# Kernel optimization log

Hardware: AMD Instinct MI355X
Metric: run time of the kernel (lower is better)

Reference implementation:

```python
import jax, jax.numpy as jnp
import numpy as np

IN_FEATURES = 4096
OUT_FEATURES = 4096
KERNEL_SIZE = 4  # MaxPool1d stride defaults to kernel_size
SCALE = 0.5


def setup_inputs() -> dict:
    key = jax.random.key(0)
    kx, kw, kb = jax.random.split(key, 3)
    bound = 1.0 / np.sqrt(IN_FEATURES)
    x = jax.random.normal(kx, (4096, IN_FEATURES), dtype=jnp.float32)
    W = jax.random.uniform(kw, (OUT_FEATURES, IN_FEATURES), dtype=jnp.float32, minval=-bound, maxval=bound)
    b = jax.random.uniform(kb, (OUT_FEATURES,), dtype=jnp.float32, minval=-bound, maxval=bound)
    return {"x": x, "W": W, "b": b}


def reference(x, W, b) -> jnp.ndarray:
    # Linear: [B, I] @ [I, O] + [O] -> [B, O]
    y = jnp.einsum("bi,oi->bo", x, W) + b
    B, O = y.shape
    K = KERNEL_SIZE
    n_win = (O - K) // K + 1  # stride == kernel_size, no padding
    # Non-overlapping window max-pool: [B, n_win, K] -> max over K
    pooled = y[:, : n_win * K].reshape(B, n_win, K).max(axis=-1)
    # Sum over pooled dim, then scale -> [B]
    return pooled.sum(axis=-1) * SCALE
```

## Files before the change

### kernel.cpp

```cpp
#include <hip/hip_runtime.h>
#include <hip/hip_bf16.h>

#define KDIM 4096
#define NTILE 64
#define NELEM16 (1u << 24)

typedef float f32x4 __attribute__((ext_vector_type(4)));
typedef short bf16x8 __attribute__((ext_vector_type(8)));

typedef const __attribute__((address_space(1))) unsigned int g_u32;
typedef __attribute__((address_space(3))) unsigned int l_u32;

__device__ __forceinline__ void gload_lds16(const void* g, void* l) {
    __builtin_amdgcn_global_load_lds((g_u32*)g, (l_u32*)l, 16, 0, 0);
}

__device__ __forceinline__ unsigned int pack_bf16x2(float lo, float hi) {
    __hip_bfloat162 h = __float22bfloat162_rn(float2{lo, hi});
    union { __hip_bfloat162 h; unsigned int u; } c; c.h = h; return c.u;
}

__global__ __launch_bounds__(256)
void pack_swz(const float* __restrict__ in, unsigned short* __restrict__ out)
{
    const unsigned int stride = gridDim.x * blockDim.x;
    for (unsigned int i = blockIdx.x * blockDim.x + threadIdx.x; i < (1u << 21); i += stride) {
        const unsigned int cp = i & 7;
        const unsigned int rl = (i >> 3) & 127;
        const unsigned int c  = cp ^ (rl & 7);
        const unsigned int h  = (i >> 10) & 1;
        const unsigned int kt = (i >> 11) & 63;
        const unsigned int rt = i >> 17;
        const unsigned int row = rt * 256 + h * 128 + rl;
        const unsigned int col = kt * 64 + c * 8;
        const float4* s = (const float4*)(in + (size_t)row * KDIM + col);
        const float4 a = s[0], b = s[1];
        uint4 o;
        o.x = pack_bf16x2(a.x, a.y); o.y = pack_bf16x2(a.z, a.w);
        o.z = pack_bf16x2(b.x, b.y); o.w = pack_bf16x2(b.z, b.w);
        *(uint4*)(out + (size_t)i * 8) = o;
    }
}

#define STAGE(matBase, kt, h, bufp, opIdx)                                      \
    {                                                                           \
        const unsigned short* g_ = (matBase) + ((size_t)(kt) * 2 + (h)) * 8192; \
        const unsigned int lo_ = (bufp) * 32768 + (opIdx) * 16384 + (h) * 8192 + wid * 1024; \
        gload_lds16(g_ + stageOff,       &lds[lo_]);                            \
        gload_lds16(g_ + stageOff + 512, &lds[lo_ + 512]);                      \
    }

#define PHASE(P, MFB, NFB, STAGE_STMT, VMSTMT)                                  \
    {                                                                           \
        bf16x8 af[4][2], bfr[2][2];                                             \
        _Pragma("unroll") for (int m = 0; m < 2; ++m)                           \
          _Pragma("unroll") for (int k = 0; k < 2; ++k)                         \
            af[m][k] = *(const bf16x8*)&lds[(P) * 32768 + (((MFB) + m) >> 2) * 8192 + \
                ((((MFB) + m) & 3) * 2 + wm) * 1024 + rdBase + kcp[k]];         \
        _Pragma("unroll") for (int m = 2; m < 4; ++m)                           \
          _Pragma("unroll") for (int k = 0; k < 2; ++k)                         \
            af[m][k] = *(const bf16x8*)&lds[(P) * 32768 + (((MFB) + m) >> 2) * 8192 + \
                ((((MFB) + m) & 3) * 2 + wm) * 1024 + rdBase + kcp[k]];         \
        _Pragma("unroll") for (int n = 0; n < 2; ++n)                           \
          _Pragma("unroll") for (int k = 0; k < 2; ++k)                         \
            bfr[n][k] = *(const bf16x8*)&lds[(P) * 32768 + 16384 +              \
                (((NFB) + n) >> 1) * 8192 + ((((NFB) + n) & 1) * 4 + wn) * 1024 + rdBase + kcp[k]]; \
        STAGE_STMT;                                                             \
        __builtin_amdgcn_s_barrier();                                           \
        __builtin_amdgcn_s_setprio(1);                                          \
        _Pragma("unroll") for (int m = 0; m < 4; ++m)                           \
          _Pragma("unroll") for (int n = 0; n < 2; ++n)                         \
            _Pragma("unroll") for (int k = 0; k < 2; ++k)                       \
              acc[(MFB) + m][(NFB) + n] = __builtin_amdgcn_mfma_f32_16x16x32_bf16( \
                  af[m][k], bfr[n][k], acc[(MFB) + m][(NFB) + n], 0, 0, 0);     \
        __builtin_amdgcn_s_setprio(0);                                          \
        VMSTMT;                                                                 \
        __builtin_amdgcn_s_barrier();                                           \
    }

__global__ __launch_bounds__(512, 2)
void gemm_8phase(const unsigned short* __restrict__ A,
                 const unsigned short* __restrict__ B,
                 const float* __restrict__ bias,
                 float* __restrict__ out)
{
    __shared__ unsigned short lds[65536];

    const int tid  = threadIdx.x;
    const int lane = tid & 63;
    const int wid  = tid >> 6;
    const int wm   = wid >> 2;
    const int wn   = wid & 3;
    const int c15  = lane & 15;
    const int q4   = lane >> 4;
    const int c7   = c15 & 7;

    const int bid = blockIdx.x;
    const int wg  = (bid & 7) * 32 + (bid >> 3);
    const int bm  = wg >> 4;
    const int bn  = wg & 15;

    const unsigned short* Abase = A + (size_t)bm * 64 * 2 * 8192;
    const unsigned short* Bbase = B + (size_t)bn * 64 * 2 * 8192;

    const int stageOff = wid * 1024 + lane * 8;
    const int rdBase   = c15 * 64;
    const int kcp[2]   = { ((0 + q4) ^ c7) * 8, ((4 + q4) ^ c7) * 8 };

    f32x4 acc[8][4];
    #pragma unroll
    for (int i = 0; i < 8; ++i)
        #pragma unroll
        for (int j = 0; j < 4; ++j)
            acc[i][j] = (f32x4)0.0f;

    STAGE(Abase, 0, 0, 0, 0);
    STAGE(Abase, 0, 1, 0, 0);
    STAGE(Bbase, 0, 0, 0, 1);
    STAGE(Bbase, 0, 1, 0, 1);
    STAGE(Bbase, 1, 0, 1, 1);
    STAGE(Abase, 1, 1, 1, 0);
    asm volatile("s_waitcnt vmcnt(4)" ::: "memory");
    __builtin_amdgcn_s_barrier();

    #pragma unroll 2
    for (int t = 0; t < NTILE; ++t) {
        const int p = t & 1;
        PHASE(p, 0, 0, if (t + 1 < NTILE) STAGE(Abase, t + 1, 0, p ^ 1, 0), );
        PHASE(p, 4, 0, if (t + 1 < NTILE) STAGE(Bbase, t + 1, 1, p ^ 1, 1), );
        PHASE(p, 4, 2, if (t + 2 < NTILE) STAGE(Bbase, t + 2, 0, p, 1), );
        PHASE(p, 0, 2, if (t + 2 < NTILE) STAGE(Abase, t + 2, 1, p, 0),
              if (t < NTILE - 2) { asm volatile("s_waitcnt vmcnt(4)" ::: "memory"); }
              else               { asm volatile("s_waitcnt vmcnt(0)" ::: "memory"); });
    }

    float rs[8][4];
    #pragma unroll
    for (int mf = 0; mf < 8; ++mf)
        #pragma unroll
        for (int r = 0; r < 4; ++r)
            rs[mf][r] = 0.0f;

    #pragma unroll
    for (int nf = 0; nf < 4; ++nf) {
        const float bv = bias[bn * 256 + (nf * 4 + wn) * 16 + c15];
        #pragma unroll
        for (int mf = 0; mf < 8; ++mf) {
            #pragma unroll
            for (int r = 0; r < 4; ++r) {
                float v = acc[mf][nf][r] + bv;
                v = fmaxf(v, __shfl_xor(v, 1));
                v = fmaxf(v, __shfl_xor(v, 2));
                v += __shfl_xor(v, 4);
                v += __shfl_xor(v, 8);
                rs[mf][r] += v;
            }
        }
    }

    if (c15 == 0) {
        #pragma unroll
        for (int mf = 0; mf < 8; ++mf)
            #pragma unroll
            for (int r = 0; r < 4; ++r) {
                const int row = bm * 256 + (mf * 2 + wm) * 16 + q4 * 4 + r;
                atomicAdd(&out[row], 0.5f * rs[mf][r]);
            }
    }
}

__global__ __launch_bounds__(256, 2)
void fused_gemm_pool_fallback(const float* __restrict__ x,
                              const float* __restrict__ W,
                              const float* __restrict__ b,
                              float* __restrict__ out)
{
    __shared__ unsigned short As[128][72];
    __shared__ unsigned short Bs[128][72];

    const int tid  = threadIdx.x;
    const int lane = tid & 63;
    const int wid  = tid >> 6;
    const int wm   = wid >> 1;
    const int wn   = wid & 1;

    const int bid = blockIdx.x;
    const int wg  = (bid & 7) * 128 + (bid >> 3);
    const int bm  = wg >> 5;
    const int bn  = wg & 31;

    const int srow = tid >> 4;
    const int scol = tid & 15;

    const float* xbase = x + (size_t)(bm * 128 + srow) * KDIM + scol * 4;
    const float* wbase = W + (size_t)(bn * 128 + srow) * KDIM + scol * 4;

    f32x4 acc[4][4];
    #pragma unroll
    for (int i = 0; i < 4; ++i)
        #pragma unroll
        for (int j = 0; j < 4; ++j)
            acc[i][j] = (f32x4)0.0f;

    float4 ra[8], rb[8];
    #pragma unroll
    for (int p = 0; p < 8; ++p) {
        ra[p] = *(const float4*)(xbase + (size_t)(p * 16) * KDIM);
        rb[p] = *(const float4*)(wbase + (size_t)(p * 16) * KDIM);
    }

    for (int kt = 0; kt < KDIM / 64; ++kt) {
        #pragma unroll
        for (int p = 0; p < 8; ++p) {
            const int r = srow + p * 16;
            uint2 pa, pb;
            pa.x = pack_bf16x2(ra[p].x, ra[p].y);
            pa.y = pack_bf16x2(ra[p].z, ra[p].w);
            pb.x = pack_bf16x2(rb[p].x, rb[p].y);
            pb.y = pack_bf16x2(rb[p].z, rb[p].w);
            *(uint2*)&As[r][scol * 4] = pa;
            *(uint2*)&Bs[r][scol * 4] = pb;
        }
        __syncthreads();

        if (kt + 1 < KDIM / 64) {
            const float* xa = xbase + (size_t)(kt + 1) * 64;
            const float* wa = wbase + (size_t)(kt + 1) * 64;
            #pragma unroll
            for (int p = 0; p < 8; ++p) {
                ra[p] = *(const float4*)(xa + (size_t)(p * 16) * KDIM);
                rb[p] = *(const float4*)(wa + (size_t)(p * 16) * KDIM);
            }
        }

        #pragma unroll
        for (int k0 = 0; k0 < 2; ++k0) {
            const int kk = k0 * 32 + (lane >> 4) * 8;
            bf16x8 af[4], bfr[4];
            #pragma unroll
            for (int mf = 0; mf < 4; ++mf)
                af[mf] = *(const bf16x8*)&As[wm * 64 + mf * 16 + (lane & 15)][kk];
            #pragma unroll
            for (int nf = 0; nf < 4; ++nf)
                bfr[nf] = *(const bf16x8*)&Bs[wn * 64 + nf * 16 + (lane & 15)][kk];
            #pragma unroll
            for (int mf = 0; mf < 4; ++mf)
                #pragma unroll
                for (int nf = 0; nf < 4; ++nf)
                    acc[mf][nf] = __builtin_amdgcn_mfma_f32_16x16x32_bf16(
                        af[mf], bfr[nf], acc[mf][nf], 0, 0, 0);
        }
        __syncthreads();
    }

    float rs[4][4];
    #pragma unroll
    for (int mf = 0; mf < 4; ++mf)
        #pragma unroll
        for (int r = 0; r < 4; ++r)
            rs[mf][r] = 0.0f;

    #pragma unroll
    for (int nf = 0; nf < 4; ++nf) {
        const float bv = b[bn * 128 + wn * 64 + nf * 16 + (lane & 15)];
        #pragma unroll
        for (int mf = 0; mf < 4; ++mf) {
            #pragma unroll
            for (int r = 0; r < 4; ++r) {
                float v = acc[mf][nf][r] + bv;
                v = fmaxf(v, __shfl_xor(v, 1));
                v = fmaxf(v, __shfl_xor(v, 2));
                v += __shfl_xor(v, 4);
                v += __shfl_xor(v, 8);
                rs[mf][r] += v;
            }
        }
    }

    if ((lane & 15) == 0) {
        #pragma unroll
        for (int mf = 0; mf < 4; ++mf)
            #pragma unroll
            for (int r = 0; r < 4; ++r) {
                const int row = bm * 128 + wm * 64 + mf * 16 + (lane >> 4) * 4 + r;
                atomicAdd(&out[row], 0.5f * rs[mf][r]);
            }
    }
}

extern "C" void kernel_launch(void* const* d_in, const int* in_sizes, int n_in,
                              void* d_out, int out_size, void* d_ws, size_t ws_size,
                              hipStream_t stream) {
    const float* x = (const float*)d_in[0];
    const float* W = (const float*)d_in[1];
    const float* b = (const float*)d_in[2];
    float* out = (float*)d_out;

    hipMemsetAsync(out, 0, (size_t)out_size * sizeof(float), stream);

    const size_t need = (size_t)NELEM16 * 2 * sizeof(unsigned short);
    if (ws_size >= need) {
        unsigned short* xb = (unsigned short*)d_ws;
        unsigned short* wb = xb + (size_t)NELEM16;
        pack_swz<<<dim3(2048), dim3(256), 0, stream>>>(x, xb);
        pack_swz<<<dim3(2048), dim3(256), 0, stream>>>(W, wb);
        gemm_8phase<<<dim3(256), dim3(512), 0, stream>>>(xb, wb, b, out);
    } else {
        fused_gemm_pool_fallback<<<dim3(1024), dim3(256), 0, stream>>>(x, W, b, out);
    }
}
```

Baseline: 187.9 us.

## Reuse LDS fragments across GEMM phases and fuse the two pack kernels

The four-phase main loop now keeps A and B fragments in registers across phases, so each phase loads only one new operand half (A0+B0, then B1, then A1, then nothing) instead of reloading both A and B every phase. This cuts LDS read traffic per tile and the matching waits. The x and W bf16 pack kernels are merged into a single launch, saving one launch and its tail. The catch is more live vector registers for the fragments under a 512-thread, 2-block launch bound, which risks spills or lower occupancy.

```diff
diff --git a/kernel.cpp b/kernel.cpp
--- a/kernel.cpp
+++ b/kernel.cpp
@@ -21,16 +21,20 @@
 }
 
 __global__ __launch_bounds__(256)
-void pack_swz(const float* __restrict__ in, unsigned short* __restrict__ out)
+void pack_swz2(const float* __restrict__ x, const float* __restrict__ W,
+               unsigned short* __restrict__ xb, unsigned short* __restrict__ wb)
 {
     const unsigned int stride = gridDim.x * blockDim.x;
-    for (unsigned int i = blockIdx.x * blockDim.x + threadIdx.x; i < (1u << 21); i += stride) {
-        const unsigned int cp = i & 7;
-        const unsigned int rl = (i >> 3) & 127;
+    for (unsigned int i = blockIdx.x * blockDim.x + threadIdx.x; i < (1u << 22); i += stride) {
+        const unsigned int j  = i & ((1u << 21) - 1);
+        const float* __restrict__ in = (i >> 21) ? W : x;
+        unsigned short* __restrict__ out = (i >> 21) ? wb : xb;
+        const unsigned int cp = j & 7;
+        const unsigned int rl = (j >> 3) & 127;
         const unsigned int c  = cp ^ (rl & 7);
-        const unsigned int h  = (i >> 10) & 1;
-        const unsigned int kt = (i >> 11) & 63;
-        const unsigned int rt = i >> 17;
+        const unsigned int h  = (j >> 10) & 1;
+        const unsigned int kt = (j >> 11) & 63;
+        const unsigned int rt = j >> 17;
         const unsigned int row = rt * 256 + h * 128 + rl;
         const unsigned int col = kt * 64 + c * 8;
         const float4* s = (const float4*)(in + (size_t)row * KDIM + col);
@@ -38,7 +42,7 @@
         uint4 o;
         o.x = pack_bf16x2(a.x, a.y); o.y = pack_bf16x2(a.z, a.w);
         o.z = pack_bf16x2(b.x, b.y); o.w = pack_bf16x2(b.z, b.w);
-        *(uint4*)(out + (size_t)i * 8) = o;
+        *(uint4*)(out + (size_t)j * 8) = o;
     }
 }
 
@@ -48,34 +52,6 @@
         const unsigned int lo_ = (bufp) * 32768 + (opIdx) * 16384 + (h) * 8192 + wid * 1024; \
         gload_lds16(g_ + stageOff,       &lds[lo_]);                            \
         gload_lds16(g_ + stageOff + 512, &lds[lo_ + 512]);                      \
-    }
-
-#define PHASE(P, MFB, NFB, STAGE_STMT, VMSTMT)                                  \
-    {                                                                           \
-        bf16x8 af[4][2], bfr[2][2];                                             \
-        _Pragma("unroll") for (int m = 0; m < 2; ++m)                           \
-          _Pragma("unroll") for (int k = 0; k < 2; ++k)                         \
-            af[m][k] = *(const bf16x8*)&lds[(P) * 32768 + (((MFB) + m) >> 2) * 8192 + \
-                ((((MFB) + m) & 3) * 2 + wm) * 1024 + rdBase + kcp[k]];         \
-        _Pragma("unroll") for (int m = 2; m < 4; ++m)                           \
-          _Pragma("unroll") for (int k = 0; k < 2; ++k)                         \
-            af[m][k] = *(const bf16x8*)&lds[(P) * 32768 + (((MFB) + m) >> 2) * 8192 + \
-                ((((MFB) + m) & 3) * 2 + wm) * 1024 + rdBase + kcp[k]];         \
-        _Pragma("unroll") for (int n = 0; n < 2; ++n)                           \
-          _Pragma("unroll") for (int k = 0; k < 2; ++k)                         \
-            bfr[n][k] = *(const bf16x8*)&lds[(P) * 32768 + 16384 +              \
-                (((NFB) + n) >> 1) * 8192 + ((((NFB) + n) & 1) * 4 + wn) * 1024 + rdBase + kcp[k]]; \
-        STAGE_STMT;                                                             \
-        __builtin_amdgcn_s_barrier();                                           \
-        __builtin_amdgcn_s_setprio(1);                                          \
-        _Pragma("unroll") for (int m = 0; m < 4; ++m)                           \
-          _Pragma("unroll") for (int n = 0; n < 2; ++n)                         \
-            _Pragma("unroll") for (int k = 0; k < 2; ++k)                       \
-              acc[(MFB) + m][(NFB) + n] = __builtin_amdgcn_mfma_f32_16x16x32_bf16( \
-                  af[m][k], bfr[n][k], acc[(MFB) + m][(NFB) + n], 0, 0, 0);     \
-        __builtin_amdgcn_s_setprio(0);                                          \
-        VMSTMT;                                                                 \
-        __builtin_amdgcn_s_barrier();                                           \
     }
 
 __global__ __launch_bounds__(512, 2)
@@ -114,6 +90,10 @@
         for (int j = 0; j < 4; ++j)
             acc[i][j] = (f32x4)0.0f;
 
+    bf16x8 afr[4][2];
+    bf16x8 b0f[2][2];
+    bf16x8 b1f[2][2];
+
     STAGE(Abase, 0, 0, 0, 0);
     STAGE(Abase, 0, 1, 0, 0);
     STAGE(Bbase, 0, 0, 0, 1);
@@ -125,13 +105,86 @@
 
     #pragma unroll 2
     for (int t = 0; t < NTILE; ++t) {
-        const int p = t & 1;
-        PHASE(p, 0, 0, if (t + 1 < NTILE) STAGE(Abase, t + 1, 0, p ^ 1, 0), );
-        PHASE(p, 4, 0, if (t + 1 < NTILE) STAGE(Bbase, t + 1, 1, p ^ 1, 1), );
-        PHASE(p, 4, 2, if (t + 2 < NTILE) STAGE(Bbase, t + 2, 0, p, 1), );
-        PHASE(p, 0, 2, if (t + 2 < NTILE) STAGE(Abase, t + 2, 1, p, 0),
-              if (t < NTILE - 2) { asm volatile("s_waitcnt vmcnt(4)" ::: "memory"); }
-              else               { asm volatile("s_waitcnt vmcnt(0)" ::: "memory"); });
+        const int p  = t & 1;
+        const int pb = p * 32768;
+
+        #pragma unroll
+        for (int m = 0; m < 4; ++m)
+            #pragma unroll
+            for (int k = 0; k < 2; ++k)
+                afr[m][k] = *(const bf16x8*)&lds[pb + (m * 2 + wm) * 1024 + rdBase + kcp[k]];
+        #pragma unroll
+        for (int n = 0; n < 2; ++n)
+            #pragma unroll
+            for (int k = 0; k < 2; ++k)
+                b0f[n][k] = *(const bf16x8*)&lds[pb + 16384 + (n * 4 + wn) * 1024 + rdBase + kcp[k]];
+        if (t + 1 < NTILE) STAGE(Abase, t + 1, 0, p ^ 1, 0);
+        __builtin_amdgcn_s_barrier();
+        __builtin_amdgcn_s_setprio(1);
+        #pragma unroll
+        for (int m = 0; m < 4; ++m)
+            #pragma unroll
+            for (int n = 0; n < 2; ++n)
+                #pragma unroll
+                for (int k = 0; k < 2; ++k)
+                    acc[m][n] = __builtin_amdgcn_mfma_f32_16x16x32_bf16(
+                        afr[m][k], b0f[n][k], acc[m][n], 0, 0, 0);
+        __builtin_amdgcn_s_setprio(0);
+        __builtin_amdgcn_s_barrier();
+
+        #pragma unroll
+        for (int n = 0; n < 2; ++n)
+            #pragma unroll
+            for (int k = 0; k < 2; ++k)
+                b1f[n][k] = *(const bf16x8*)&lds[pb + 16384 + 8192 + (n * 4 + wn) * 1024 + rdBase + kcp[k]];
+        if (t + 1 < NTILE) STAGE(Bbase, t + 1, 1, p ^ 1, 1);
+        __builtin_amdgcn_s_barrier();
+        __builtin_amdgcn_s_setprio(1);
+        #pragma unroll
+        for (int m = 0; m < 4; ++m)
+            #pragma unroll
+            for (int n = 0; n < 2; ++n)
+                #pragma unroll
+                for (int k = 0; k < 2; ++k)
+                    acc[m][2 + n] = __builtin_amdgcn_mfma_f32_16x16x32_bf16(
+                        afr[m][k], b1f[n][k], acc[m][2 + n], 0, 0, 0);
+        __builtin_amdgcn_s_setprio(0);
+        __builtin_amdgcn_s_barrier();
+
+        #pragma unroll
+        for (int m = 0; m < 4; ++m)
+            #pragma unroll
+            for (int k = 0; k < 2; ++k)
+                afr[m][k] = *(const bf16x8*)&lds[pb + 8192 + (m * 2 + wm) * 1024 + rdBase + kcp[k]];
+        if (t + 2 < NTILE) STAGE(Bbase, t + 2, 0, p, 1);
+        __builtin_amdgcn_s_barrier();
+        __builtin_amdgcn_s_setprio(1);
+        #pragma unroll
+        for (int m = 0; m < 4; ++m)
+            #pragma unroll
+            for (int n = 0; n < 2; ++n)
+                #pragma unroll
+                for (int k = 0; k < 2; ++k)
+                    acc[4 + m][2 + n] = __builtin_amdgcn_mfma_f32_16x16x32_bf16(
+                        afr[m][k], b1f[n][k], acc[4 + m][2 + n], 0, 0, 0);
+        __builtin_amdgcn_s_setprio(0);
+        __builtin_amdgcn_s_barrier();
+
+        if (t + 2 < NTILE) STAGE(Abase, t + 2, 1, p, 0);
+        __builtin_amdgcn_s_barrier();
+        __builtin_amdgcn_s_setprio(1);
+        #pragma unroll
+        for (int m = 0; m < 4; ++m)
+            #pragma unroll
+            for (int n = 0; n < 2; ++n)
+                #pragma unroll
+                for (int k = 0; k < 2; ++k)
+                    acc[4 + m][n] = __builtin_amdgcn_mfma_f32_16x16x32_bf16(
+                        afr[m][k], b0f[n][k], acc[4 + m][n], 0, 0, 0);
+        __builtin_amdgcn_s_setprio(0);
+        if (t < NTILE - 2) { asm volatile("s_waitcnt vmcnt(4)" ::: "memory"); }
+        else               { asm volatile("s_waitcnt vmcnt(0)" ::: "memory"); }
+        __builtin_amdgcn_s_barrier();
     }
 
     float rs[8][4];
@@ -302,8 +355,7 @@
     if (ws_size >= need) {
         unsigned short* xb = (unsigned short*)d_ws;
         unsigned short* wb = xb + (size_t)NELEM16;
-        pack_swz<<<dim3(2048), dim3(256), 0, stream>>>(x, xb);
-        pack_swz<<<dim3(2048), dim3(256), 0, stream>>>(W, wb);
+        pack_swz2<<<dim3(2048), dim3(256), 0, stream>>>(x, W, xb, wb);
         gemm_8phase<<<dim3(256), dim3(512), 0, stream>>>(xb, wb, b, out);
     } else {
         fused_gemm_pool_fallback<<<dim3(1024), dim3(256), 0, stream>>>(x, W, b, out);
```

After: 170.9 us. 1.1x faster.

## Software-pipeline LDS fragment reads across phases and merge pack kernels

Applied to the files above, without the earlier changes.

Restructures the GEMM main loop so LDS fragment reads for the next phase are issued before the current phase's MFMAs. Fragment registers are double-buffered (aA/aB, b0A/b0B), fine-grained lgkmcnt waits and sched_barriers are used, and the prefetch distance of global-to-LDS staging changes to two tiles ahead. This aims to hide LDS read latency behind matrix work. It also fuses the two bf16 pack launches into one kernel to save a launch. The trade-off is higher register pressure and tricky buffer-reuse correctness.

```diff
diff --git a/kernel.cpp b/kernel.cpp
--- a/kernel.cpp
+++ b/kernel.cpp
@@ -21,16 +21,20 @@
 }
 
 __global__ __launch_bounds__(256)
-void pack_swz(const float* __restrict__ in, unsigned short* __restrict__ out)
+void pack_swz2(const float* __restrict__ x, const float* __restrict__ W,
+               unsigned short* __restrict__ xb, unsigned short* __restrict__ wb)
 {
     const unsigned int stride = gridDim.x * blockDim.x;
-    for (unsigned int i = blockIdx.x * blockDim.x + threadIdx.x; i < (1u << 21); i += stride) {
-        const unsigned int cp = i & 7;
-        const unsigned int rl = (i >> 3) & 127;
+    for (unsigned int i = blockIdx.x * blockDim.x + threadIdx.x; i < (1u << 22); i += stride) {
+        const unsigned int j  = i & ((1u << 21) - 1);
+        const float* __restrict__ in = (i >> 21) ? W : x;
+        unsigned short* __restrict__ out = (i >> 21) ? wb : xb;
+        const unsigned int cp = j & 7;
+        const unsigned int rl = (j >> 3) & 127;
         const unsigned int c  = cp ^ (rl & 7);
-        const unsigned int h  = (i >> 10) & 1;
-        const unsigned int kt = (i >> 11) & 63;
-        const unsigned int rt = i >> 17;
+        const unsigned int h  = (j >> 10) & 1;
+        const unsigned int kt = (j >> 11) & 63;
+        const unsigned int rt = j >> 17;
         const unsigned int row = rt * 256 + h * 128 + rl;
         const unsigned int col = kt * 64 + c * 8;
         const float4* s = (const float4*)(in + (size_t)row * KDIM + col);
@@ -38,7 +42,7 @@
         uint4 o;
         o.x = pack_bf16x2(a.x, a.y); o.y = pack_bf16x2(a.z, a.w);
         o.z = pack_bf16x2(b.x, b.y); o.w = pack_bf16x2(b.z, b.w);
-        *(uint4*)(out + (size_t)i * 8) = o;
+        *(uint4*)(out + (size_t)j * 8) = o;
     }
 }
 
@@ -50,31 +54,60 @@
         gload_lds16(g_ + stageOff + 512, &lds[lo_ + 512]);                      \
     }
 
-#define PHASE(P, MFB, NFB, STAGE_STMT, VMSTMT)                                  \
+#define READ_A(dst, base)                                                       \
+    _Pragma("unroll") for (int m = 0; m < 4; ++m)                               \
+      _Pragma("unroll") for (int k = 0; k < 2; ++k)                             \
+        dst[m][k] = *(const bf16x8*)&lds[(base) + (m * 2 + wm) * 1024 + rdBase + kcp[k]];
+
+#define READ_B(dst, base)                                                       \
+    _Pragma("unroll") for (int n = 0; n < 2; ++n)                               \
+      _Pragma("unroll") for (int k = 0; k < 2; ++k)                             \
+        dst[n][k] = *(const bf16x8*)&lds[(base) + (n * 4 + wn) * 1024 + rdBase + kcp[k]];
+
+#define MFMA16(AF, BF, MO, NO)                                                  \
+    __builtin_amdgcn_s_setprio(1);                                              \
+    _Pragma("unroll") for (int m = 0; m < 4; ++m)                               \
+      _Pragma("unroll") for (int n = 0; n < 2; ++n)                             \
+        _Pragma("unroll") for (int k = 0; k < 2; ++k)                           \
+          acc[(MO) + m][(NO) + n] = __builtin_amdgcn_mfma_f32_16x16x32_bf16(    \
+              AF[m][k], BF[n][k], acc[(MO) + m][(NO) + n], 0, 0, 0);            \
+    __builtin_amdgcn_s_setprio(0);
+
+#define TILE_BODY(t, PB, B0CUR, B0NXT)                                          \
     {                                                                           \
-        bf16x8 af[4][2], bfr[2][2];                                             \
-        _Pragma("unroll") for (int m = 0; m < 2; ++m)                           \
-          _Pragma("unroll") for (int k = 0; k < 2; ++k)                         \
-            af[m][k] = *(const bf16x8*)&lds[(P) * 32768 + (((MFB) + m) >> 2) * 8192 + \
-                ((((MFB) + m) & 3) * 2 + wm) * 1024 + rdBase + kcp[k]];         \
-        _Pragma("unroll") for (int m = 2; m < 4; ++m)                           \
-          _Pragma("unroll") for (int k = 0; k < 2; ++k)                         \
-            af[m][k] = *(const bf16x8*)&lds[(P) * 32768 + (((MFB) + m) >> 2) * 8192 + \
-                ((((MFB) + m) & 3) * 2 + wm) * 1024 + rdBase + kcp[k]];         \
-        _Pragma("unroll") for (int n = 0; n < 2; ++n)                           \
-          _Pragma("unroll") for (int k = 0; k < 2; ++k)                         \
-            bfr[n][k] = *(const bf16x8*)&lds[(P) * 32768 + 16384 +              \
-                (((NFB) + n) >> 1) * 8192 + ((((NFB) + n) & 1) * 4 + wn) * 1024 + rdBase + kcp[k]]; \
-        STAGE_STMT;                                                             \
-        __builtin_amdgcn_s_barrier();                                           \
-        __builtin_amdgcn_s_setprio(1);                                          \
-        _Pragma("unroll") for (int m = 0; m < 4; ++m)                           \
-          _Pragma("unroll") for (int n = 0; n < 2; ++n)                         \
-            _Pragma("unroll") for (int k = 0; k < 2; ++k)                       \
-              acc[(MFB) + m][(NFB) + n] = __builtin_amdgcn_mfma_f32_16x16x32_bf16( \
-                  af[m][k], bfr[n][k], acc[(MFB) + m][(NFB) + n], 0, 0, 0);     \
-        __builtin_amdgcn_s_setprio(0);                                          \
-        VMSTMT;                                                                 \
+                                                                        \
+        READ_B(b1, (PB) + 16384 + 8192);                                        \
+        asm volatile("s_waitcnt lgkmcnt(4)" ::: "memory");                      \
+        __builtin_amdgcn_sched_barrier(0);                                      \
+        if ((t) + 2 < NTILE) STAGE(Abase, (t) + 2, 0, (PB) ? 1 : 0, 0);         \
+        __builtin_amdgcn_s_barrier();                                           \
+        MFMA16(aA, B0CUR, 0, 0);                                                \
+        __builtin_amdgcn_s_barrier();                                           \
+                                                                        \
+        READ_A(aB, (PB) + 8192);                                                \
+        asm volatile("s_waitcnt lgkmcnt(8)" ::: "memory");                      \
+        __builtin_amdgcn_sched_barrier(0);                                      \
+        if ((t) + 2 < NTILE) STAGE(Bbase, (t) + 2, 0, (PB) ? 1 : 0, 1);         \
+        __builtin_amdgcn_s_barrier();                                           \
+        MFMA16(aA, b1, 0, 2);                                                   \
+        __builtin_amdgcn_s_barrier();                                           \
+                                                                        \
+        READ_A(aA, (PB) ^ 32768);                                               \
+        asm volatile("s_waitcnt lgkmcnt(8)" ::: "memory");                      \
+        __builtin_amdgcn_sched_barrier(0);                                      \
+        if ((t) + 2 < NTILE) STAGE(Bbase, (t) + 2, 1, (PB) ? 1 : 0, 1);         \
+        __builtin_amdgcn_s_barrier();                                           \
+        MFMA16(aB, b1, 4, 2);                                                   \
+        __builtin_amdgcn_s_barrier();                                           \
+                                                                        \
+        READ_B(B0NXT, ((PB) ^ 32768) + 16384);                                  \
+        asm volatile("s_waitcnt lgkmcnt(4)" ::: "memory");                      \
+        __builtin_amdgcn_sched_barrier(0);                                      \
+        if ((t) + 2 < NTILE) STAGE(Abase, (t) + 2, 1, (PB) ? 1 : 0, 0);         \
+        __builtin_amdgcn_s_barrier();                                           \
+        MFMA16(aB, B0CUR, 4, 0);                                                \
+        if ((t) < NTILE - 2)       { asm volatile("s_waitcnt vmcnt(4)" ::: "memory"); } \
+        else if ((t) == NTILE - 2) { asm volatile("s_waitcnt vmcnt(0)" ::: "memory"); } \
         __builtin_amdgcn_s_barrier();                                           \
     }
 
@@ -114,24 +147,29 @@
         for (int j = 0; j < 4; ++j)
             acc[i][j] = (f32x4)0.0f;
 
+    bf16x8 aA[4][2];
+    bf16x8 aB[4][2];
+    bf16x8 b1[2][2];
+    bf16x8 b0A[2][2];
+    bf16x8 b0B[2][2];
+
     STAGE(Abase, 0, 0, 0, 0);
-    STAGE(Abase, 0, 1, 0, 0);
     STAGE(Bbase, 0, 0, 0, 1);
     STAGE(Bbase, 0, 1, 0, 1);
+    STAGE(Abase, 0, 1, 0, 0);
+    STAGE(Abase, 1, 0, 1, 0);
     STAGE(Bbase, 1, 0, 1, 1);
+    STAGE(Bbase, 1, 1, 1, 1);
     STAGE(Abase, 1, 1, 1, 0);
     asm volatile("s_waitcnt vmcnt(4)" ::: "memory");
     __builtin_amdgcn_s_barrier();
 
-    #pragma unroll 2
-    for (int t = 0; t < NTILE; ++t) {
-        const int p = t & 1;
-        PHASE(p, 0, 0, if (t + 1 < NTILE) STAGE(Abase, t + 1, 0, p ^ 1, 0), );
-        PHASE(p, 4, 0, if (t + 1 < NTILE) STAGE(Bbase, t + 1, 1, p ^ 1, 1), );
-        PHASE(p, 4, 2, if (t + 2 < NTILE) STAGE(Bbase, t + 2, 0, p, 1), );
-        PHASE(p, 0, 2, if (t + 2 < NTILE) STAGE(Abase, t + 2, 1, p, 0),
-              if (t < NTILE - 2) { asm volatile("s_waitcnt vmcnt(4)" ::: "memory"); }
-              else               { asm volatile("s_waitcnt vmcnt(0)" ::: "memory"); });
+    READ_A(aA,  0);
+    READ_B(b0A, 16384);
+
+    for (int tt = 0; tt < NTILE; tt += 2) {
+        TILE_BODY(tt,     0,     b0A, b0B);
+        TILE_BODY(tt + 1, 32768, b0B, b0A);
     }
 
     float rs[8][4];
@@ -302,8 +340,7 @@
     if (ws_size >= need) {
         unsigned short* xb = (unsigned short*)d_ws;
         unsigned short* wb = xb + (size_t)NELEM16;
-        pack_swz<<<dim3(2048), dim3(256), 0, stream>>>(x, xb);
-        pack_swz<<<dim3(2048), dim3(256), 0, stream>>>(W, wb);
+        pack_swz2<<<dim3(2048), dim3(256), 0, stream>>>(x, W, xb, wb);
         gemm_8phase<<<dim3(256), dim3(512), 0, stream>>>(xb, wb, b, out);
     } else {
         fused_gemm_pool_fallback<<<dim3(1024), dim3(256), 0, stream>>>(x, W, b, out);
```

Result: slower. 195.0 us (+3.8%).

## Pre-pack operands in MFMA fragment order and load directly to registers, dropping LDS

Applied to the files above, without the earlier changes.

The pack kernel now writes x and W in the exact per-lane MFMA fragment order and handles both matrices in one launch. The GEMM drops LDS staging and barriers entirely: each wave loads its fragments straight from global memory into registers, double-buffered across K half-tiles. This removes LDS traffic and synchronisation, but each wave now fetches its own A/B fragments from global/L2 with less data reuse across waves. Register pressure also rises, and occupancy is reduced to one block per CU.

```diff
diff --git a/kernel.cpp b/kernel.cpp
--- a/kernel.cpp
+++ b/kernel.cpp
@@ -8,84 +8,58 @@
 typedef float f32x4 __attribute__((ext_vector_type(4)));
 typedef short bf16x8 __attribute__((ext_vector_type(8)));
 
-typedef const __attribute__((address_space(1))) unsigned int g_u32;
-typedef __attribute__((address_space(3))) unsigned int l_u32;
-
-__device__ __forceinline__ void gload_lds16(const void* g, void* l) {
-    __builtin_amdgcn_global_load_lds((g_u32*)g, (l_u32*)l, 16, 0, 0);
-}
-
 __device__ __forceinline__ unsigned int pack_bf16x2(float lo, float hi) {
     __hip_bfloat162 h = __float22bfloat162_rn(float2{lo, hi});
     union { __hip_bfloat162 h; unsigned int u; } c; c.h = h; return c.u;
 }
 
 __global__ __launch_bounds__(256)
-void pack_swz(const float* __restrict__ in, unsigned short* __restrict__ out)
+void pack_frag2(const float* __restrict__ x, const float* __restrict__ W,
+                unsigned short* __restrict__ xb, unsigned short* __restrict__ wb)
 {
     const unsigned int stride = gridDim.x * blockDim.x;
-    for (unsigned int i = blockIdx.x * blockDim.x + threadIdx.x; i < (1u << 21); i += stride) {
-        const unsigned int cp = i & 7;
-        const unsigned int rl = (i >> 3) & 127;
-        const unsigned int c  = cp ^ (rl & 7);
-        const unsigned int h  = (i >> 10) & 1;
-        const unsigned int kt = (i >> 11) & 63;
-        const unsigned int rt = i >> 17;
-        const unsigned int row = rt * 256 + h * 128 + rl;
-        const unsigned int col = kt * 64 + c * 8;
-        const float4* s = (const float4*)(in + (size_t)row * KDIM + col);
-        const float4 a = s[0], b = s[1];
+    for (unsigned int i = blockIdx.x * blockDim.x + threadIdx.x; i < (1u << 22); i += stride) {
+        const unsigned int j  = i & ((1u << 21) - 1);
+        const float* __restrict__ in = (i >> 21) ? W : x;
+        unsigned short* __restrict__ out = (i >> 21) ? wb : xb;
+        const unsigned int lane = j & 63;
+        const unsigned int s    = (j >> 6) & 1;
+        const unsigned int f    = (j >> 7) & 15;
+        const unsigned int kt   = (j >> 11) & 63;
+        const unsigned int t    = j >> 17;
+        const unsigned int row  = t * 256 + f * 16 + (lane & 15);
+        const unsigned int col  = kt * 64 + s * 32 + (lane >> 4) * 8;
+        const float4* sp = (const float4*)(in + (size_t)row * KDIM + col);
+        const float4 a = sp[0], b = sp[1];
         uint4 o;
         o.x = pack_bf16x2(a.x, a.y); o.y = pack_bf16x2(a.z, a.w);
         o.z = pack_bf16x2(b.x, b.y); o.w = pack_bf16x2(b.z, b.w);
-        *(uint4*)(out + (size_t)i * 8) = o;
-    }
-}
-
-#define STAGE(matBase, kt, h, bufp, opIdx)                                      \
-    {                                                                           \
-        const unsigned short* g_ = (matBase) + ((size_t)(kt) * 2 + (h)) * 8192; \
-        const unsigned int lo_ = (bufp) * 32768 + (opIdx) * 16384 + (h) * 8192 + wid * 1024; \
-        gload_lds16(g_ + stageOff,       &lds[lo_]);                            \
-        gload_lds16(g_ + stageOff + 512, &lds[lo_ + 512]);                      \
-    }
-
-#define PHASE(P, MFB, NFB, STAGE_STMT, VMSTMT)                                  \
-    {                                                                           \
-        bf16x8 af[4][2], bfr[2][2];                                             \
-        _Pragma("unroll") for (int m = 0; m < 2; ++m)                           \
-          _Pragma("unroll") for (int k = 0; k < 2; ++k)                         \
-            af[m][k] = *(const bf16x8*)&lds[(P) * 32768 + (((MFB) + m) >> 2) * 8192 + \
-                ((((MFB) + m) & 3) * 2 + wm) * 1024 + rdBase + kcp[k]];         \
-        _Pragma("unroll") for (int m = 2; m < 4; ++m)                           \
-          _Pragma("unroll") for (int k = 0; k < 2; ++k)                         \
-            af[m][k] = *(const bf16x8*)&lds[(P) * 32768 + (((MFB) + m) >> 2) * 8192 + \
-                ((((MFB) + m) & 3) * 2 + wm) * 1024 + rdBase + kcp[k]];         \
-        _Pragma("unroll") for (int n = 0; n < 2; ++n)                           \
-          _Pragma("unroll") for (int k = 0; k < 2; ++k)                         \
-            bfr[n][k] = *(const bf16x8*)&lds[(P) * 32768 + 16384 +              \
-                (((NFB) + n) >> 1) * 8192 + ((((NFB) + n) & 1) * 4 + wn) * 1024 + rdBase + kcp[k]]; \
-        STAGE_STMT;                                                             \
-        __builtin_amdgcn_s_barrier();                                           \
-        __builtin_amdgcn_s_setprio(1);                                          \
-        _Pragma("unroll") for (int m = 0; m < 4; ++m)                           \
-          _Pragma("unroll") for (int n = 0; n < 2; ++n)                         \
-            _Pragma("unroll") for (int k = 0; k < 2; ++k)                       \
-              acc[(MFB) + m][(NFB) + n] = __builtin_amdgcn_mfma_f32_16x16x32_bf16( \
-                  af[m][k], bfr[n][k], acc[(MFB) + m][(NFB) + n], 0, 0, 0);     \
-        __builtin_amdgcn_s_setprio(0);                                          \
-        VMSTMT;                                                                 \
-        __builtin_amdgcn_s_barrier();                                           \
-    }
-
-__global__ __launch_bounds__(512, 2)
-void gemm_8phase(const unsigned short* __restrict__ A,
-                 const unsigned short* __restrict__ B,
-                 const float* __restrict__ bias,
-                 float* __restrict__ out)
+        *(uint4*)(out + (size_t)j * 8) = o;
+    }
+}
+
+#define LOADS(AB, BB, t, s)                                                     \
+    _Pragma("unroll") for (int m = 0; m < 8; ++m)                               \
+        AB[m] = *(const bf16x8*)&Ab[(size_t)(t) * 16384 +                       \
+            (((m * 2 + wm) * 2 + (s)) * 512) + lane * 8];                       \
+    _Pragma("unroll") for (int n = 0; n < 4; ++n)                               \
+        BB[n] = *(const bf16x8*)&Bb[(size_t)(t) * 16384 +                       \
+            (((n * 4 + wn) * 2 + (s)) * 512) + lane * 8];
+
+#define MFMAH(AB, BB)                                                           \
+    __builtin_amdgcn_s_setprio(1);                                              \
+    _Pragma("unroll") for (int m = 0; m < 8; ++m)                               \
+      _Pragma("unroll") for (int n = 0; n < 4; ++n)                             \
+        acc[m][n] = __builtin_amdgcn_mfma_f32_16x16x32_bf16(                    \
+            AB[m], BB[n], acc[m][n], 0, 0, 0);                                  \
+    __builtin_amdgcn_s_setprio(0);
+
+__global__ __launch_bounds__(512, 1)
+void gemm_nolds(const unsigned short* __restrict__ A,
+                const unsigned short* __restrict__ B,
+                const float* __restrict__ bias,
+                float* __restrict__ out)
 {
-    __shared__ unsigned short lds[65536];
-
     const int tid  = threadIdx.x;
     const int lane = tid & 63;
     const int wid  = tid >> 6;
@@ -93,19 +67,14 @@
     const int wn   = wid & 3;
     const int c15  = lane & 15;
     const int q4   = lane >> 4;
-    const int c7   = c15 & 7;
 
     const int bid = blockIdx.x;
     const int wg  = (bid & 7) * 32 + (bid >> 3);
     const int bm  = wg >> 4;
     const int bn  = wg & 15;
 
-    const unsigned short* Abase = A + (size_t)bm * 64 * 2 * 8192;
-    const unsigned short* Bbase = B + (size_t)bn * 64 * 2 * 8192;
-
-    const int stageOff = wid * 1024 + lane * 8;
-    const int rdBase   = c15 * 64;
-    const int kcp[2]   = { ((0 + q4) ^ c7) * 8, ((4 + q4) ^ c7) * 8 };
+    const unsigned short* Ab = A + ((size_t)bm << 20);
+    const unsigned short* Bb = B + ((size_t)bn << 20);
 
     f32x4 acc[8][4];
     #pragma unroll
@@ -114,24 +83,16 @@
         for (int j = 0; j < 4; ++j)
             acc[i][j] = (f32x4)0.0f;
 
-    STAGE(Abase, 0, 0, 0, 0);
-    STAGE(Abase, 0, 1, 0, 0);
-    STAGE(Bbase, 0, 0, 0, 1);
-    STAGE(Bbase, 0, 1, 0, 1);
-    STAGE(Bbase, 1, 0, 1, 1);
-    STAGE(Abase, 1, 1, 1, 0);
-    asm volatile("s_waitcnt vmcnt(4)" ::: "memory");
-    __builtin_amdgcn_s_barrier();
-
-    #pragma unroll 2
+    bf16x8 aX[8], bX[4];
+    bf16x8 aY[8], bY[4];
+
+    LOADS(aX, bX, 0, 0);
+
     for (int t = 0; t < NTILE; ++t) {
-        const int p = t & 1;
-        PHASE(p, 0, 0, if (t + 1 < NTILE) STAGE(Abase, t + 1, 0, p ^ 1, 0), );
-        PHASE(p, 4, 0, if (t + 1 < NTILE) STAGE(Bbase, t + 1, 1, p ^ 1, 1), );
-        PHASE(p, 4, 2, if (t + 2 < NTILE) STAGE(Bbase, t + 2, 0, p, 1), );
-        PHASE(p, 0, 2, if (t + 2 < NTILE) STAGE(Abase, t + 2, 1, p, 0),
-              if (t < NTILE - 2) { asm volatile("s_waitcnt vmcnt(4)" ::: "memory"); }
-              else               { asm volatile("s_waitcnt vmcnt(0)" ::: "memory"); });
+        LOADS(aY, bY, t, 1);
+        MFMAH(aX, bX);
+        if (t + 1 < NTILE) { LOADS(aX, bX, t + 1, 0); }
+        MFMAH(aY, bY);
     }
 
     float rs[8][4];
@@ -302,9 +263,8 @@
     if (ws_size >= need) {
         unsigned short* xb = (unsigned short*)d_ws;
         unsigned short* wb = xb + (size_t)NELEM16;
-        pack_swz<<<dim3(2048), dim3(256), 0, stream>>>(x, xb);
-        pack_swz<<<dim3(2048), dim3(256), 0, stream>>>(W, wb);
-        gemm_8phase<<<dim3(256), dim3(512), 0, stream>>>(xb, wb, b, out);
+        pack_frag2<<<dim3(2048), dim3(256), 0, stream>>>(x, W, xb, wb);
+        gemm_nolds<<<dim3(256), dim3(512), 0, stream>>>(xb, wb, b, out);
     } else {
         fused_gemm_pool_fallback<<<dim3(1024), dim3(256), 0, stream>>>(x, W, b, out);
     }
```

Measured after the change: 184.8 us. About the same (-1.6%).
